# Performance work log

Hardware: AMD Instinct MI355X
Metric: run time of the kernel (lower is better)

Reference implementation:

```python
import jax, jax.numpy as jnp
import numpy as np

N = 40000          # nodes
E = 640000         # edges (avg degree 16)
D_MODEL = 128
H = 8              # num_heads
DH = 16            # d_head
DFF = 512
CLAMP = 5.0
EPS = 1e-5


def setup_inputs() -> dict:
    key = jax.random.key(0)
    ks = jax.random.split(key, 10)
    s = 0.08  # weight init scale
    return {
        "feat": jax.random.normal(ks[0], (N, D_MODEL), dtype=jnp.float32),
        "src": jax.random.randint(ks[1], (E,), 0, N, dtype=jnp.int32),
        "dst": jax.random.randint(ks[2], (E,), 0, N, dtype=jnp.int32),
        "Wq": jax.random.normal(ks[3], (H * DH, D_MODEL), dtype=jnp.float32) * s,
        "Wk": jax.random.normal(ks[4], (H * DH, D_MODEL), dtype=jnp.float32) * s,
        "Wv": jax.random.normal(ks[5], (H * DH, D_MODEL), dtype=jnp.float32) * s,
        "Wo": jax.random.normal(ks[6], (D_MODEL, H * DH), dtype=jnp.float32) * s,
        "ln1_g": jnp.ones((D_MODEL,), jnp.float32),
        "ln1_b": jnp.zeros((D_MODEL,), jnp.float32),
        "W1": jax.random.normal(ks[7], (DFF, D_MODEL), dtype=jnp.float32) * s,
        "b1": jnp.zeros((DFF,), jnp.float32),
        "W2": jax.random.normal(ks[8], (D_MODEL, DFF), dtype=jnp.float32) * s,
        "b2": jnp.zeros((D_MODEL,), jnp.float32),
        "ln2_g": jnp.ones((D_MODEL,), jnp.float32),
        "ln2_b": jnp.zeros((D_MODEL,), jnp.float32),
    }


def _layer_norm(x, g, b):
    mu = jnp.mean(x, axis=-1, keepdims=True)
    var = jnp.mean(jnp.square(x - mu), axis=-1, keepdims=True)
    return (x - mu) * jax.lax.rsqrt(var + EPS) * g + b


def reference(feat, src, dst, Wq, Wk, Wv, Wo, ln1_g, ln1_b, W1, b1, W2, b2, ln2_g, ln2_b):
    n = feat.shape[0]
    # Node-level projections (equivalent to DGL's per-edge Linear on gathered feats)
    q = (feat @ Wq.T).reshape(n, H, DH)
    k = (feat @ Wk.T).reshape(n, H, DH)
    v = (feat @ Wv.T).reshape(n, H, DH)

    # Per-edge multi-head attention logits: q[dst] . k[src] / sqrt(d_head), clamped
    u = jnp.sum(q[dst] * k[src], axis=-1) / np.sqrt(DH)   # [E, H]
    u = jnp.clip(u, -CLAMP, CLAMP)

    # Ragged edge-softmax over incoming edges of each dst node
    m = jax.ops.segment_max(u, dst, num_segments=n)        # [N, H]
    e = jnp.exp(u - m[dst])                                # [E, H]
    denom = jax.ops.segment_sum(e, dst, num_segments=n)    # [N, H]
    a = e / denom[dst]                                     # [E, H]

    # Weighted V scatter-reduce back to dst nodes
    av = (a[:, :, None] * v[src]).reshape(-1, H * DH)      # [E, H*DH]
    sum_av = jax.ops.segment_sum(av, dst, num_segments=n)  # [N, H*DH]
    uh = sum_av @ Wo.T                                     # [N, d_model]

    h1 = _layer_norm(feat + uh, ln1_g, ln1_b)
    ffn = jax.nn.relu(h1 @ W1.T + b1) @ W2.T + b2
    return _layer_norm(h1 + ffn, ln2_g, ln2_b)
```

## Files before the change

### kernel.cpp

```cpp
#include <hip/hip_runtime.h>

#define DM 128
#define DFF 512
#define CLAMP_V 5.0f
#define LN_EPS 1e-5f

typedef __attribute__((ext_vector_type(8))) short bf16x8;
typedef __attribute__((ext_vector_type(4))) float f32x4;

__device__ __forceinline__ float b2f(ushort u) {
  union { uint u; float f; } x; x.u = ((uint)u) << 16; return x.f;
}
__device__ __forceinline__ ushort f2b(float f) {
  union { float f; uint u; } x; x.f = f;
  uint r = x.u + 0x7FFFu + ((x.u >> 16) & 1u);
  return (ushort)(r >> 16);
}
__device__ __forceinline__ void unpackw(uint w, float& lo, float& hi) {
  union { uint u; float f; } A, B;
  A.u = w << 16; B.u = w & 0xFFFF0000u;
  lo = A.f; hi = B.f;
}
__device__ __forceinline__ void unpack8w(uint4 w, float* o) {
  unpackw(w.x, o[0], o[1]); unpackw(w.y, o[2], o[3]);
  unpackw(w.z, o[4], o[5]); unpackw(w.w, o[6], o[7]);
}

__global__ void k_prep(const float* __restrict__ feat,
                       const float* __restrict__ wq, const float* __restrict__ wk,
                       const float* __restrict__ wv, const float* __restrict__ wo,
                       const float* __restrict__ w1, const float* __restrict__ w2,
                       ushort* __restrict__ feat_bf, ushort* __restrict__ wbf,
                       const int* __restrict__ dst, int* __restrict__ deg,
                       int nf4, int castBlocks, int E) {
  if ((int)blockIdx.x >= castBlocks) {
    int e = ((int)blockIdx.x - castBlocks) * 256 + threadIdx.x;
    if (e < E) atomicAdd(&deg[dst[e]], 1);
    return;
  }
  int i = blockIdx.x * 256 + threadIdx.x;
  if (i < nf4) {
    float4 v = *reinterpret_cast<const float4*>(feat + i * 4);
    ushort4 o; o.x = f2b(v.x); o.y = f2b(v.y); o.z = f2b(v.z); o.w = f2b(v.w);
    *reinterpret_cast<ushort4*>(feat_bf + i * 4) = o;
    return;
  }
  int i4 = (i - nf4) * 4;
  if (i4 >= 196608) return;
  const float* s; int o;
  if      (i4 < 16384)  { s = wq; o = i4; }
  else if (i4 < 32768)  { s = wk; o = i4 - 16384; }
  else if (i4 < 49152)  { s = wv; o = i4 - 32768; }
  else if (i4 < 65536)  { s = wo; o = i4 - 49152; }
  else if (i4 < 131072) { s = w1; o = i4 - 65536; }
  else                  { s = w2; o = i4 - 131072; }
  float4 v = *reinterpret_cast<const float4*>(s + o);
  ushort4 u; u.x = f2b(v.x); u.y = f2b(v.y); u.z = f2b(v.z); u.w = f2b(v.w);
  *reinterpret_cast<ushort4*>(wbf + i4) = u;
}

#define SC_EPB 1024

__global__ __launch_bounds__(256) void k_scan1(const int* __restrict__ deg,
                                               int* __restrict__ off,
                                               int* __restrict__ bsum, int n) {
  __shared__ int sh[256];
  const int t = threadIdx.x;
  int base = blockIdx.x * SC_EPB + t * 4;
  int4 v = {0, 0, 0, 0};
  if (base + 3 < n) {
    v = *reinterpret_cast<const int4*>(deg + base);
  } else {
    if (base     < n) v.x = deg[base];
    if (base + 1 < n) v.y = deg[base + 1];
    if (base + 2 < n) v.z = deg[base + 2];
    if (base + 3 < n) v.w = deg[base + 3];
  }
  int s = v.x + v.y + v.z + v.w;
  sh[t] = s;
  __syncthreads();
  #pragma unroll
  for (int d = 1; d < 256; d <<= 1) {
    int x = 0;
    if (t >= d) x = sh[t - d];
    __syncthreads();
    sh[t] += x;
    __syncthreads();
  }
  int ex = sh[t] - s;
  if (base + 3 < n) {
    int4 o; o.x = ex; o.y = ex + v.x; o.z = ex + v.x + v.y; o.w = ex + v.x + v.y + v.z;
    *reinterpret_cast<int4*>(off + base) = o;
  } else {
    if (base     < n) off[base]     = ex;
    if (base + 1 < n) off[base + 1] = ex + v.x;
    if (base + 2 < n) off[base + 2] = ex + v.x + v.y;
    if (base + 3 < n) off[base + 3] = ex + v.x + v.y + v.z;
  }
  if (t == 255) bsum[blockIdx.x] = sh[255];
}

__global__ __launch_bounds__(256) void k_scan3(int* __restrict__ off,
                                               const int* __restrict__ bsum,
                                               int nbk, int n, int E) {
  __shared__ int sadd;
  const int t = threadIdx.x;
  if (t < 64) {
    int v = (t < nbk && t < (int)blockIdx.x) ? bsum[t] : 0;
    #pragma unroll
    for (int msk = 1; msk < 64; msk <<= 1) v += __shfl_xor(v, msk);
    if (t == 0) sadd = v;
  }
  __syncthreads();
  int add = sadd;
  int base = blockIdx.x * SC_EPB + t * 4;
  if (base + 3 < n) {
    int4 v = *reinterpret_cast<int4*>(off + base);
    v.x += add; v.y += add; v.z += add; v.w += add;
    *reinterpret_cast<int4*>(off + base) = v;
  } else {
    if (base     < n) off[base]     += add;
    if (base + 1 < n) off[base + 1] += add;
    if (base + 2 < n) off[base + 2] += add;
  }
  if (blockIdx.x == 0 && t == 0) off[n] = E;
}

__global__ void k_scatter(const int* __restrict__ src, const int* __restrict__ dst,
                          const int* __restrict__ off, int* __restrict__ cur,
                          int* __restrict__ csr, int E) {
  int e = blockIdx.x * blockDim.x + threadIdx.x;
  if (e < E) {
    int d = dst[e];
    int p = off[d] + atomicAdd(&cur[d], 1);
    csr[p] = src[e];
  }
}

template<int FLAGS, bool QKVSPLIT, bool OUTF, bool OUTB>
__global__ __launch_bounds__(512, 2) void k_mmT(
    const ushort* __restrict__ A, const ushort* __restrict__ W,
    const float* __restrict__ bias, const float* __restrict__ res,
    const float* __restrict__ lng, const float* __restrict__ lnbv,
    float* __restrict__ Cf, ushort* __restrict__ Cb, ushort* __restrict__ Cb2,
    int M, int ldc)
{
  __shared__ ushort As[128 * 128];
  __shared__ ushort Bs[128 * 128];
  __shared__ float lnred[(FLAGS & 8) ? 1024 : 4];

  const int tid = threadIdx.x;
  const int wv = tid >> 6, ln = tid & 63;
  const int bnb = blockIdx.x;
  const int mbase = blockIdx.y * 128;
  const int wrow = (wv >> 2) * 64, wcol = (wv & 3) * 32;
  const int o_base = tid * 16;

  #pragma unroll
  for (int is = 0; is < 4; ++is) {
    int o = is * 8192 + o_base;
    int row = o >> 8;
    int c = ((o >> 4) & 15) ^ (row & 15);
    int gr = min(mbase + row, M - 1);
    const ushort* sA = A + (size_t)gr * 128 + c * 8;
    __builtin_amdgcn_global_load_lds(
        (const __attribute__((address_space(1))) void*)sA,
        (__attribute__((address_space(3))) void*)((char*)As + is * 8192 + wv * 1024),
        16, 0, 0);
    const ushort* sB = W + (size_t)(bnb * 128 + row) * 128 + c * 8;
    __builtin_amdgcn_global_load_lds(
        (const __attribute__((address_space(1))) void*)sB,
        (__attribute__((address_space(3))) void*)((char*)Bs + is * 8192 + wv * 1024),
        16, 0, 0);
  }
  __syncthreads();

  f32x4 acc[4][2] = {};
  const char* AsB = (const char*)As;
  const char* BsB = (const char*)Bs;
  #pragma unroll
  for (int kk = 0; kk < 4; ++kk) {
    bf16x8 af[4], bfr[2];
    #pragma unroll
    for (int m = 0; m < 4; ++m) {
      int r = wrow + m * 16 + (ln & 15);
      int c = kk * 4 + (ln >> 4);
      af[m] = *reinterpret_cast<const bf16x8*>(AsB + r * 256 + ((c ^ (r & 15)) << 4));
    }
    #pragma unroll
    for (int n = 0; n < 2; ++n) {
      int r = wcol + n * 16 + (ln & 15);
      int c = kk * 4 + (ln >> 4);
      bfr[n] = *reinterpret_cast<const bf16x8*>(BsB + r * 256 + ((c ^ (r & 15)) << 4));
    }
    #pragma unroll
    for (int m = 0; m < 4; ++m)
      #pragma unroll
      for (int n = 0; n < 2; ++n)
        acc[m][n] = __builtin_amdgcn_mfma_f32_16x16x32_bf16(af[m], bfr[n], acc[m][n], 0, 0, 0);
  }

  if constexpr ((FLAGS & 8) != 0) {
    #pragma unroll
    for (int m = 0; m < 4; ++m)
      #pragma unroll
      for (int n = 0; n < 2; ++n) {
        int gc = wcol + n * 16 + (ln & 15);
        #pragma unroll
        for (int r = 0; r < 4; ++r) {
          int gr = mbase + wrow + m * 16 + (ln >> 4) * 4 + r;
          float v = acc[m][n][r];
          if (FLAGS & 1) v += bias[gc];
          if (FLAGS & 2) v = fmaxf(v, 0.f);
          if (FLAGS & 4) v += res[(size_t)min(gr, M - 1) * 128 + gc];
          acc[m][n][r] = v;
        }
      }
    #pragma unroll
    for (int m = 0; m < 4; ++m)
      #pragma unroll
      for (int r = 0; r < 4; ++r) {
        float sm = acc[m][0][r] + acc[m][1][r];
        float sq = acc[m][0][r] * acc[m][0][r] + acc[m][1][r] * acc[m][1][r];
        #pragma unroll
        for (int msk = 1; msk <= 8; msk <<= 1) {
          sm += __shfl_xor(sm, msk);
          sq += __shfl_xor(sq, msk);
        }
        if ((ln & 15) == 0) {
          int row = wrow + m * 16 + (ln >> 4) * 4 + r;
          lnred[row * 8 + (wv & 3) * 2]     = sm;
          lnred[row * 8 + (wv & 3) * 2 + 1] = sq;
        }
      }
    __syncthreads();
    #pragma unroll
    for (int m = 0; m < 4; ++m)
      #pragma unroll
      for (int r = 0; r < 4; ++r) {
        int row = wrow + m * 16 + (ln >> 4) * 4 + r;
        int gr = mbase + row;
        float sm = lnred[row * 8] + lnred[row * 8 + 2] + lnred[row * 8 + 4] + lnred[row * 8 + 6];
        float sq = lnred[row * 8 + 1] + lnred[row * 8 + 3] + lnred[row * 8 + 5] + lnred[row * 8 + 7];
        float mu = sm * (1.f / 128.f);
        float var = fmaxf(sq * (1.f / 128.f) - mu * mu, 0.f);
        float rstd = rsqrtf(var + LN_EPS);
        if (gr < M) {
          #pragma unroll
          for (int n = 0; n < 2; ++n) {
            int gc = wcol + n * 16 + (ln & 15);
            float y = (acc[m][n][r] - mu) * rstd * lng[gc] + lnbv[gc];
            if (OUTF) Cf[(size_t)gr * 128 + gc] = y;
            if (OUTB) Cb[(size_t)gr * 128 + gc] = f2b(y);
          }
        }
      }
  } else {
    #pragma unroll
    for (int m = 0; m < 4; ++m) {
      int gr0 = mbase + wrow + m * 16 + (ln >> 4) * 4;
      #pragma unroll
      for (int n = 0; n < 2; ++n) {
        int gcl = wcol + n * 16 + (ln & 15);
        float bsv = (FLAGS & 1) ? bias[bnb * 128 + gcl] : 0.f;
        #pragma unroll
        for (int r = 0; r < 4; ++r) {
          int gr = gr0 + r;
          if (gr >= M) continue;
          float v = acc[m][n][r] + bsv;
          if (FLAGS & 2) v = fmaxf(v, 0.f);
          if (QKVSPLIT) {
            if (bnb == 0) Cb[(size_t)gr * 128 + gcl] = f2b(v);
            else          Cb2[(size_t)gr * 256 + (bnb - 1) * 128 + gcl] = f2b(v);
          } else {
            if (OUTF) Cf[(size_t)gr * ldc + bnb * 128 + gcl] = v;
            if (OUTB) Cb[(size_t)gr * ldc + bnb * 128 + gcl] = f2b(v);
          }
        }
      }
    }
  }
}

__global__ __launch_bounds__(512, 4) void k_ffn(
    const ushort* __restrict__ h1b, const float* __restrict__ h1f,
    const ushort* __restrict__ w1, const float* __restrict__ b1,
    const ushort* __restrict__ w2, const float* __restrict__ b2,
    const float* __restrict__ lng, const float* __restrict__ lnbv,
    float* __restrict__ outp, int M)
{
  __shared__ ushort mid[64 * 512];
  __shared__ float lnred[64 * 16];

  const int tid = threadIdx.x;
  const int wv = tid >> 6, ln = tid & 63;
  const int lr = ln & 15, hi = ln >> 4;
  const int mbase = blockIdx.x * 64;

  #pragma unroll
  for (int is = 0; is < 2; ++is) {
    int o = is * 8192 + tid * 16;
    int row = o >> 8;
    int c = ((o >> 4) & 15) ^ (row & 15);
    int gr = min(mbase + row, M - 1);
    const ushort* s = h1b + (size_t)gr * 128 + c * 8;
    __builtin_amdgcn_global_load_lds(
        (const __attribute__((address_space(1))) void*)s,
        (__attribute__((address_space(3))) void*)((char*)mid + is * 8192 + wv * 1024),
        16, 0, 0);
  }
  __syncthreads();

  f32x4 p1[4][4] = {};
  const char* hB = (const char*)mid;
  #pragma unroll
  for (int kk = 0; kk < 4; ++kk) {
    bf16x8 aW[4], bH[4];
    #pragma unroll
    for (int mi = 0; mi < 4; ++mi) {
      int w1row = wv * 64 + mi * 16 + lr;
      aW[mi] = *reinterpret_cast<const bf16x8*>(w1 + (size_t)w1row * 128 + kk * 32 + hi * 8);
    }
    #pragma unroll
    for (int hj = 0; hj < 4; ++hj) {
      int r = hj * 16 + lr;
      int c = kk * 4 + hi;
      bH[hj] = *reinterpret_cast<const bf16x8*>(hB + r * 256 + ((c ^ (r & 15)) << 4));
    }
    #pragma unroll
    for (int mi = 0; mi < 4; ++mi)
      #pragma unroll
      for (int hj = 0; hj < 4; ++hj)
        p1[mi][hj] = __builtin_amdgcn_mfma_f32_16x16x32_bf16(aW[mi], bH[hj], p1[mi][hj], 0, 0, 0);
  }
  __syncthreads();

  #pragma unroll
  for (int mi = 0; mi < 4; ++mi) {
    int mc0 = wv * 64 + mi * 16 + hi * 4;
    float4 bv = *reinterpret_cast<const float4*>(b1 + mc0);
    int chunk = mc0 >> 3;
    int sub = (mc0 & 7) * 2;
    #pragma unroll
    for (int hj = 0; hj < 4; ++hj) {
      int orow = hj * 16 + lr;
      ushort4 pk;
      pk.x = f2b(fmaxf(p1[mi][hj][0] + bv.x, 0.f));
      pk.y = f2b(fmaxf(p1[mi][hj][1] + bv.y, 0.f));
      pk.z = f2b(fmaxf(p1[mi][hj][2] + bv.z, 0.f));
      pk.w = f2b(fmaxf(p1[mi][hj][3] + bv.w, 0.f));
      char* dstp = (char*)mid + orow * 1024 + (((chunk & 63) ^ (orow & 15)) << 4) + sub;
      *reinterpret_cast<ushort4*>(dstp) = pk;
    }
  }
  __syncthreads();

  f32x4 p2[4] = {};
  #pragma unroll
  for (int kk = 0; kk < 16; ++kk) {
    bf16x8 aM[4], bW;
    int c2 = kk * 4 + hi;
    #pragma unroll
    for (int m = 0; m < 4; ++m) {
      int r = m * 16 + lr;
      aM[m] = *reinterpret_cast<const bf16x8*>((const char*)mid + r * 1024 + ((c2 ^ (r & 15)) << 4));
    }
    int w2row = wv * 16 + lr;
    bW = *reinterpret_cast<const bf16x8*>(w2 + (size_t)w2row * 512 + kk * 32 + hi * 8);
    #pragma unroll
    for (int m = 0; m < 4; ++m)
      p2[m] = __builtin_amdgcn_mfma_f32_16x16x32_bf16(aM[m], bW, p2[m], 0, 0, 0);
  }

  {
    int gc = wv * 16 + lr;
    float bsv = b2[gc];
    #pragma unroll
    for (int m = 0; m < 4; ++m)
      #pragma unroll
      for (int r = 0; r < 4; ++r) {
        int gr = mbase + m * 16 + hi * 4 + r;
        p2[m][r] += bsv + h1f[(size_t)min(gr, M - 1) * 128 + gc];
      }
  }
  #pragma unroll
  for (int m = 0; m < 4; ++m)
    #pragma unroll
    for (int r = 0; r < 4; ++r) {
      float sm = p2[m][r];
      float sq = p2[m][r] * p2[m][r];
      #pragma unroll
      for (int msk = 1; msk <= 8; msk <<= 1) {
        sm += __shfl_xor(sm, msk);
        sq += __shfl_xor(sq, msk);
      }
      if (lr == 0) {
        int row = m * 16 + hi * 4 + r;
        lnred[row * 16 + wv * 2]     = sm;
        lnred[row * 16 + wv * 2 + 1] = sq;
      }
    }
  __syncthreads();
  #pragma unroll
  for (int m = 0; m < 4; ++m)
    #pragma unroll
    for (int r = 0; r < 4; ++r) {
      int row = m * 16 + hi * 4 + r;
      int gr = mbase + row;
      float sm = 0.f, sq = 0.f;
      #pragma unroll
      for (int w = 0; w < 8; ++w) {
        sm += lnred[row * 16 + w * 2];
        sq += lnred[row * 16 + w * 2 + 1];
      }
      float mu = sm * (1.f / 128.f);
      float var = fmaxf(sq * (1.f / 128.f) - mu * mu, 0.f);
      float rstd = rsqrtf(var + LN_EPS);
      if (gr < M) {
        int gc = wv * 16 + lr;
        outp[(size_t)gr * 128 + gc] = (p2[m][r] - mu) * rstd * lng[gc] + lnbv[gc];
      }
    }
}

__global__ __launch_bounds__(256) void k_attn(
    const ushort* __restrict__ q, const ushort* __restrict__ kv,
    const int* __restrict__ off, const int* __restrict__ csr,
    ushort* __restrict__ sav, int n)
{
  int node = blockIdx.x * 4 + (threadIdx.x >> 6);
  int lane = threadIdx.x & 63;
  if (node >= n) return;
  const int g = lane >> 3, sl = lane & 7;

  const ushort* qr = q + (size_t)node * 128 + sl * 16;
  uint4 qw0 = *reinterpret_cast<const uint4*>(qr);
  uint4 qw1 = *reinterpret_cast<const uint4*>(qr + 8);
  float qv[16];
  unpack8w(qw0, qv); unpack8w(qw1, qv + 8);

  int b = off[node], e = off[node + 1];
  float s = 0.f;
  float a[16] = {};
  int nIt = (e - b + 7) >> 3;
  int idx = b + g;
  int sn = (b < e) ? csr[min(idx, e - 1)] : 0;

  for (int i = 0; i < nIt; ++i) {
    bool act = idx < e;
    const ushort* kr = kv + (size_t)sn * 256 + sl * 16;
    uint4 kw0 = *reinterpret_cast<const uint4*>(kr);
    uint4 kw1 = *reinterpret_cast<const uint4*>(kr + 8);
    uint4 vw0 = *reinterpret_cast<const uint4*>(kr + 128);
    uint4 vw1 = *reinterpret_cast<const uint4*>(kr + 136);
    idx += 8;
    if (i + 1 < nIt) sn = csr[min(idx, e - 1)];

    float kk[16];
    unpack8w(kw0, kk); unpack8w(kw1, kk + 8);
    float p = 0.f;
    #pragma unroll
    for (int j = 0; j < 16; ++j) p = fmaf(qv[j], kk[j], p);
    float u = fminf(fmaxf(p * 0.25f, -CLAMP_V), CLAMP_V);
    float w = __expf(u - CLAMP_V);
    w = act ? w : 0.f;
    s += w;
    float vvv[16];
    unpack8w(vw0, vvv); unpack8w(vw1, vvv + 8);
    #pragma unroll
    for (int j = 0; j < 16; ++j) a[j] = fmaf(w, vvv[j], a[j]);
  }

  #pragma unroll
  for (int msk = 8; msk <= 32; msk <<= 1) {
    s += __shfl_xor(s, msk);
    #pragma unroll
    for (int j = 0; j < 16; ++j) a[j] += __shfl_xor(a[j], msk);
  }

  float inv = (s > 0.f) ? 1.f / s : 0.f;
  if (g == 0) {
    uint w[8];
    #pragma unroll
    for (int j = 0; j < 8; ++j)
      w[j] = (uint)f2b(a[2 * j] * inv) | ((uint)f2b(a[2 * j + 1] * inv) << 16);
    ushort* outp = sav + (size_t)node * 128 + sl * 16;
    uint4 o0 = {w[0], w[1], w[2], w[3]};
    uint4 o1 = {w[4], w[5], w[6], w[7]};
    *reinterpret_cast<uint4*>(outp) = o0;
    *reinterpret_cast<uint4*>(outp + 8) = o1;
  }
}

extern "C" void kernel_launch(void* const* d_in, const int* in_sizes, int n_in,
                              void* d_out, int out_size, void* d_ws, size_t ws_size,
                              hipStream_t stream)
{
  const float* feat = (const float*)d_in[0];
  const int*   src  = (const int*)d_in[1];
  const int*   dst  = (const int*)d_in[2];
  const float* Wq   = (const float*)d_in[3];
  const float* Wk   = (const float*)d_in[4];
  const float* Wv   = (const float*)d_in[5];
  const float* Wo   = (const float*)d_in[6];
  const float* ln1g = (const float*)d_in[7];
  const float* ln1b = (const float*)d_in[8];
  const float* W1   = (const float*)d_in[9];
  const float* b1   = (const float*)d_in[10];
  const float* W2   = (const float*)d_in[11];
  const float* b2   = (const float*)d_in[12];
  const float* ln2g = (const float*)d_in[13];
  const float* ln2b = (const float*)d_in[14];
  float* out = (float*)d_out;

  const int N = in_sizes[0] / DM;
  const int E = in_sizes[1];
  const size_t NB = (size_t)N;

  char* wsb = (char*)d_ws;
  ushort* q_bf    = (ushort*)wsb;
  ushort* kv_bf   = (ushort*)(wsb + NB * 256);
  ushort* sav_bf  = (ushort*)(wsb + NB * 768);
  float*  h1      = (float*)(wsb + NB * 1024);
  ushort* h1b     = (ushort*)(wsb + NB * 1536);
  ushort* feat_bf = (ushort*)(wsb + NB * 1792);
  ushort* wbf     = (ushort*)(wsb + NB * 2048);
  ushort* wqkv_bf = wbf;
  ushort* wo_bf   = wbf + 49152;
  ushort* w1_bf   = wbf + 65536;
  ushort* w2_bf   = wbf + 131072;
  int* ib  = (int*)(wbf + 196608);
  int* deg = ib;
  int* cur = ib + N;
  int* off = ib + 2 * N;
  int* csr = ib + 3 * N + 1;
  int* bsum = csr + E;

  hipMemsetAsync(deg, 0, 2 * (size_t)N * sizeof(int), stream);

  int nf4 = N * DM / 4;
  int castBlocks = (nf4 + 49152 + 255) / 256;
  int cntBlocks = (E + 255) / 256;
  k_prep<<<castBlocks + cntBlocks, 256, 0, stream>>>(
      feat, Wq, Wk, Wv, Wo, W1, W2, feat_bf, wbf, dst, deg, nf4, castBlocks, E);

  int nbk = (N + SC_EPB - 1) / SC_EPB;
  k_scan1<<<nbk, 256, 0, stream>>>(deg, off, bsum, N);
  k_scan3<<<nbk, 256, 0, stream>>>(off, bsum, nbk, N, E);
  k_scatter<<<cntBlocks, 256, 0, stream>>>(src, dst, off, cur, csr, E);

  int nb4 = (N + 3) / 4;
  const int nT = (N + 127) / 128;

  k_mmT<0, true, false, true><<<dim3(3, nT), 512, 0, stream>>>(
      feat_bf, wqkv_bf, nullptr, nullptr, nullptr, nullptr,
      nullptr, q_bf, kv_bf, N, 128);

  k_attn<<<nb4, 256, 0, stream>>>(q_bf, kv_bf, off, csr, sav_bf, N);

  k_mmT<4 | 8, false, true, true><<<dim3(1, nT), 512, 0, stream>>>(
      sav_bf, wo_bf, nullptr, feat, ln1g, ln1b, h1, h1b, nullptr, N, 128);

  const int nF = (N + 63) / 64;
  k_ffn<<<nF, 512, 0, stream>>>(
      h1b, h1, w1_bf, b1, w2_bf, b2, ln2g, ln2b, out, N);
}
```

Baseline: 194.3 us.

## Stage FFN weights into double-buffered LDS via async global-to-LDS loads

The fused FFN kernel now streams W1 and W2 in 128x128 tiles into two swizzled LDS buffers with global_load_lds, prefetching the next tile while MFMAs run on the current one. Before, each wave read weight fragments straight from global memory. The W1 output mapping changes so that each wave covers 16 rows in each of four 128-column groups. LDS use grows by 64 KB per block and launch bounds drop from 4 to 2 blocks per CU, so occupancy falls. More barriers are added, and the LayerNorm reduction scratch now reuses the weight buffer.

```diff
diff --git a/kernel.cpp b/kernel.cpp
--- a/kernel.cpp
+++ b/kernel.cpp
@@ -282,7 +282,7 @@
   }
 }
 
-__global__ __launch_bounds__(512, 4) void k_ffn(
+__global__ __launch_bounds__(512, 2) void k_ffn(
     const ushort* __restrict__ h1b, const float* __restrict__ h1f,
     const ushort* __restrict__ w1, const float* __restrict__ b1,
     const ushort* __restrict__ w2, const float* __restrict__ b2,
@@ -290,54 +290,71 @@
     float* __restrict__ outp, int M)
 {
   __shared__ ushort mid[64 * 512];
-  __shared__ float lnred[64 * 16];
+  __shared__ ushort wbuf[2][128 * 128];
 
   const int tid = threadIdx.x;
   const int wv = tid >> 6, ln = tid & 63;
   const int lr = ln & 15, hi = ln >> 4;
   const int mbase = blockIdx.x * 64;
 
+  auto STG128 = [&](const ushort* srcBase, int srcLd, int colOff, ushort* dstLds) {
+    #pragma unroll
+    for (int is = 0; is < 4; ++is) {
+      int o = is * 8192 + tid * 16;
+      int r = o >> 8;
+      int c = ((o >> 4) & 15) ^ (r & 15);
+      const ushort* s = srcBase + (size_t)r * srcLd + colOff + c * 8;
+      __builtin_amdgcn_global_load_lds(
+          (const __attribute__((address_space(1))) void*)s,
+          (__attribute__((address_space(3))) void*)((char*)dstLds + is * 8192 + wv * 1024),
+          16, 0, 0);
+    }
+  };
+
   #pragma unroll
   for (int is = 0; is < 2; ++is) {
     int o = is * 8192 + tid * 16;
-    int row = o >> 8;
-    int c = ((o >> 4) & 15) ^ (row & 15);
-    int gr = min(mbase + row, M - 1);
+    int r = o >> 8;
+    int c = ((o >> 4) & 15) ^ (r & 15);
+    int gr = min(mbase + r, M - 1);
     const ushort* s = h1b + (size_t)gr * 128 + c * 8;
     __builtin_amdgcn_global_load_lds(
         (const __attribute__((address_space(1))) void*)s,
         (__attribute__((address_space(3))) void*)((char*)mid + is * 8192 + wv * 1024),
         16, 0, 0);
   }
+  STG128(w1, 128, 0, wbuf[0]);
   __syncthreads();
 
   f32x4 p1[4][4] = {};
   const char* hB = (const char*)mid;
   #pragma unroll
-  for (int kk = 0; kk < 4; ++kk) {
-    bf16x8 aW[4], bH[4];
-    #pragma unroll
-    for (int mi = 0; mi < 4; ++mi) {
-      int w1row = wv * 64 + mi * 16 + lr;
-      aW[mi] = *reinterpret_cast<const bf16x8*>(w1 + (size_t)w1row * 128 + kk * 32 + hi * 8);
-    }
-    #pragma unroll
-    for (int hj = 0; hj < 4; ++hj) {
-      int r = hj * 16 + lr;
+  for (int g = 0; g < 4; ++g) {
+    const int buf = g & 1;
+    if (g < 3) STG128(w1 + (size_t)(g + 1) * 128 * 128, 128, 0, wbuf[buf ^ 1]);
+    else       STG128(w2, 512, 0, wbuf[buf ^ 1]);
+    const char* wB = (const char*)wbuf[buf];
+    #pragma unroll
+    for (int kk = 0; kk < 4; ++kk) {
       int c = kk * 4 + hi;
-      bH[hj] = *reinterpret_cast<const bf16x8*>(hB + r * 256 + ((c ^ (r & 15)) << 4));
-    }
-    #pragma unroll
-    for (int mi = 0; mi < 4; ++mi)
+      int wr = wv * 16 + lr;
+      bf16x8 aW = *reinterpret_cast<const bf16x8*>(wB + wr * 256 + ((c ^ (wr & 15)) << 4));
+      bf16x8 bH[4];
+      #pragma unroll
+      for (int hj = 0; hj < 4; ++hj) {
+        int r = hj * 16 + lr;
+        bH[hj] = *reinterpret_cast<const bf16x8*>(hB + r * 256 + ((c ^ (r & 15)) << 4));
+      }
       #pragma unroll
       for (int hj = 0; hj < 4; ++hj)
-        p1[mi][hj] = __builtin_amdgcn_mfma_f32_16x16x32_bf16(aW[mi], bH[hj], p1[mi][hj], 0, 0, 0);
-  }
-  __syncthreads();
-
-  #pragma unroll
-  for (int mi = 0; mi < 4; ++mi) {
-    int mc0 = wv * 64 + mi * 16 + hi * 4;
+        p1[g][hj] = __builtin_amdgcn_mfma_f32_16x16x32_bf16(aW, bH[hj], p1[g][hj], 0, 0, 0);
+    }
+    __syncthreads();
+  }
+
+  #pragma unroll
+  for (int g = 0; g < 4; ++g) {
+    int mc0 = g * 128 + wv * 16 + hi * 4;
     float4 bv = *reinterpret_cast<const float4*>(b1 + mc0);
     int chunk = mc0 >> 3;
     int sub = (mc0 & 7) * 2;
@@ -345,10 +362,10 @@
     for (int hj = 0; hj < 4; ++hj) {
       int orow = hj * 16 + lr;
       ushort4 pk;
-      pk.x = f2b(fmaxf(p1[mi][hj][0] + bv.x, 0.f));
-      pk.y = f2b(fmaxf(p1[mi][hj][1] + bv.y, 0.f));
-      pk.z = f2b(fmaxf(p1[mi][hj][2] + bv.z, 0.f));
-      pk.w = f2b(fmaxf(p1[mi][hj][3] + bv.w, 0.f));
+      pk.x = f2b(fmaxf(p1[g][hj][0] + bv.x, 0.f));
+      pk.y = f2b(fmaxf(p1[g][hj][1] + bv.y, 0.f));
+      pk.z = f2b(fmaxf(p1[g][hj][2] + bv.z, 0.f));
+      pk.w = f2b(fmaxf(p1[g][hj][3] + bv.w, 0.f));
       char* dstp = (char*)mid + orow * 1024 + (((chunk & 63) ^ (orow & 15)) << 4) + sub;
       *reinterpret_cast<ushort4*>(dstp) = pk;
     }
@@ -357,21 +374,30 @@
 
   f32x4 p2[4] = {};
   #pragma unroll
-  for (int kk = 0; kk < 16; ++kk) {
-    bf16x8 aM[4], bW;
-    int c2 = kk * 4 + hi;
-    #pragma unroll
-    for (int m = 0; m < 4; ++m) {
-      int r = m * 16 + lr;
-      aM[m] = *reinterpret_cast<const bf16x8*>((const char*)mid + r * 1024 + ((c2 ^ (r & 15)) << 4));
-    }
-    int w2row = wv * 16 + lr;
-    bW = *reinterpret_cast<const bf16x8*>(w2 + (size_t)w2row * 512 + kk * 32 + hi * 8);
-    #pragma unroll
-    for (int m = 0; m < 4; ++m)
-      p2[m] = __builtin_amdgcn_mfma_f32_16x16x32_bf16(aM[m], bW, p2[m], 0, 0, 0);
-  }
-
+  for (int g2 = 0; g2 < 4; ++g2) {
+    const int buf = g2 & 1;
+    if (g2 < 3) STG128(w2, 512, (g2 + 1) * 128, wbuf[buf ^ 1]);
+    const char* wB = (const char*)wbuf[buf];
+    #pragma unroll
+    for (int kk = 0; kk < 4; ++kk) {
+      int wr = wv * 16 + lr;
+      int cw = kk * 4 + hi;
+      bf16x8 bW = *reinterpret_cast<const bf16x8*>(wB + wr * 256 + ((cw ^ (wr & 15)) << 4));
+      int cm = g2 * 16 + kk * 4 + hi;
+      bf16x8 aM[4];
+      #pragma unroll
+      for (int m = 0; m < 4; ++m) {
+        int r = m * 16 + lr;
+        aM[m] = *reinterpret_cast<const bf16x8*>((const char*)mid + r * 1024 + (((cm & 63) ^ (r & 15)) << 4));
+      }
+      #pragma unroll
+      for (int m = 0; m < 4; ++m)
+        p2[m] = __builtin_amdgcn_mfma_f32_16x16x32_bf16(aM[m], bW, p2[m], 0, 0, 0);
+    }
+    __syncthreads();
+  }
+
+  float* lnred = reinterpret_cast<float*>(&wbuf[0][0]);
   {
     int gc = wv * 16 + lr;
     float bsv = b2[gc];
```

Result: no change. 193.2 us (-0.6%).
